# Kernel optimization log

Measured on AMD Instinct MI355X. Metric: run time of the kernel, lower is better.

The kernel has to match this reference:

```python
import jax, jax.numpy as jnp
import numpy as np

DIM = 1024
HEADS = 16
HEAD_DIM = DIM // HEADS
SCALE = HEAD_DIM ** -0.5
EPS_R = 1e-8
EPS_LN = 1e-5


def setup_inputs() -> dict:
    key = jax.random.key(0)
    ks = jax.random.split(key, 8)
    B, L = 4, 2048
    tokens = jax.random.normal(ks[0], (B, L, DIM), dtype=jnp.float32)
    R = jax.random.uniform(ks[1], (L, L), dtype=jnp.float32)
    s = DIM ** -0.5
    Wq = jax.random.normal(ks[2], (DIM, DIM), dtype=jnp.float32) * s
    Wk = jax.random.normal(ks[3], (DIM, DIM), dtype=jnp.float32) * s
    Wv = jax.random.normal(ks[4], (DIM, DIM), dtype=jnp.float32) * s
    Wp = jax.random.normal(ks[5], (DIM, DIM), dtype=jnp.float32) * s
    beta = jnp.ones((1,), dtype=jnp.float32)
    gamma = jnp.ones((DIM,), dtype=jnp.float32)
    bias = jnp.zeros((DIM,), dtype=jnp.float32)
    return {"tokens": tokens, "R": R, "Wq": Wq, "Wk": Wk, "Wv": Wv,
            "Wp": Wp, "beta": beta, "gamma": gamma, "bias": bias}


def reference(tokens, R, Wq, Wk, Wv, Wp, beta, gamma, bias):
    B, L, D = tokens.shape
    H, Dh = HEADS, HEAD_DIM
    residual = tokens
    # nn.Linear(bias=False): y = x @ W.T
    Q = (tokens @ Wq.T).reshape(B, L, H, Dh).transpose(0, 2, 1, 3)  # [B,H,L,Dh]
    K = (tokens @ Wk.T).reshape(B, L, H, Dh).transpose(0, 2, 1, 3)
    V = (tokens @ Wv.T).reshape(B, L, H, Dh).transpose(0, 2, 1, 3)
    attn = jnp.einsum('bhqd,bhkd->bhqk', Q, K) * SCALE
    log_R = jnp.log(jnp.maximum(R, EPS_R))  # [L,L]
    attn = attn + beta[0] * log_R[None, None, :, :]
    attn = jax.nn.softmax(attn, axis=-1)
    out = jnp.einsum('bhqk,bhkd->bhqd', attn, V)
    out = out.transpose(0, 2, 1, 3).reshape(B, L, D)
    out = out @ Wp.T
    x = out + residual
    mu = jnp.mean(x, axis=-1, keepdims=True)
    var = jnp.mean(jnp.square(x - mu), axis=-1, keepdims=True)
    return (x - mu) * jax.lax.rsqrt(var + EPS_LN) * gamma + bias
```

## Files before the change

kernel.cpp:

```cpp
#include <hip/hip_runtime.h>

#define DEV __device__ __forceinline__

typedef __attribute__((ext_vector_type(2))) float f32x2;
typedef __attribute__((ext_vector_type(4))) float f32x4;
typedef __attribute__((ext_vector_type(16))) float f32x16;
typedef __attribute__((ext_vector_type(8))) short bf8v;
typedef __attribute__((ext_vector_type(4))) unsigned short u16x4;
typedef __attribute__((ext_vector_type(8))) unsigned short u16x8;
typedef __attribute__((ext_vector_type(2))) unsigned int u32x2;
typedef __attribute__((ext_vector_type(4))) unsigned int u32x4;

static constexpr int LSEQ = 2048;
static constexpr int DIM  = 1024;
static constexpr int NH   = 16;
static constexpr int DH   = 64;
static constexpr int NB   = 4;
static constexpr int MROWS = NB * LSEQ;
static constexpr float QSCALE = 0.18033688011112042f;

DEV unsigned short f2bf(float x) {
  unsigned u = __float_as_uint(x);
  return (unsigned short)((u + 0x7fffu + ((u >> 16) & 1u)) >> 16);
}

DEV unsigned cvt_pk_bf16(float a, float b) {
  unsigned r;
  asm("v_cvt_pk_bf16_f32 %0, %1, %2" : "=v"(r) : "v"(a), "v"(b));
  return r;
}

DEV void pl32swap(unsigned& a, unsigned& b) {
  asm("v_permlane32_swap_b32 %0, %1" : "+v"(a), "+v"(b));
}

DEV float fexp2(float x) {
  float r;
  asm("v_exp_f32 %0, %1" : "=v"(r) : "v"(x));
  return r;
}

DEV void gload_lds16(const void* g, void* l) {
  __builtin_amdgcn_global_load_lds((const __attribute__((address_space(1))) void*)g,
                                   (__attribute__((address_space(3))) void*)l, 16, 0, 0);
}

__global__ __launch_bounds__(256) void k_cvt(const float* __restrict__ src,
                                             unsigned short* __restrict__ dst, int n) {
  int i = (blockIdx.x * 256 + threadIdx.x) * 8;
  if (i >= n) return;
  f32x4 a = *(const f32x4*)(src + i);
  f32x4 b = *(const f32x4*)(src + i + 4);
  u16x8 o;
  o[0] = f2bf(a[0]); o[1] = f2bf(a[1]); o[2] = f2bf(a[2]); o[3] = f2bf(a[3]);
  o[4] = f2bf(b[0]); o[5] = f2bf(b[1]); o[6] = f2bf(b[2]); o[7] = f2bf(b[3]);
  *(u16x8*)(dst + i) = o;
}

__global__ __launch_bounds__(256) void k_cvtw(const float* __restrict__ w0,
                                              const float* __restrict__ w1,
                                              const float* __restrict__ w2,
                                              const float* __restrict__ w3,
                                              unsigned short* __restrict__ dst) {
  int r = blockIdx.x >> 9;
  const float* src = (r == 0) ? w0 : (r == 1) ? w1 : (r == 2) ? w2 : w3;
  int i = ((blockIdx.x & 511) * 256 + threadIdx.x) * 8;
  f32x4 a = *(const f32x4*)(src + i);
  f32x4 b = *(const f32x4*)(src + i + 4);
  u16x8 o;
  o[0] = f2bf(a[0]); o[1] = f2bf(a[1]); o[2] = f2bf(a[2]); o[3] = f2bf(a[3]);
  o[4] = f2bf(b[0]); o[5] = f2bf(b[1]); o[6] = f2bf(b[2]); o[7] = f2bf(b[3]);
  *(u16x8*)(dst + (size_t)r * DIM * DIM + i) = o;
}

__global__ __launch_bounds__(256) void k_rbx(const float* __restrict__ R,
                                             const float* __restrict__ beta,
                                             u16x4* __restrict__ out) {
  __shared__ u16x4 lds2[2048];
  const int tid = threadIdx.x;
  const int q0 = blockIdx.x * 128;
  const int t  = blockIdx.y;
  const float b = beta[0];
  #pragma unroll
  for (int it = 0; it < 4; ++it) {
    int ql = it * 32 + (tid >> 3);
    int kl = (tid & 7) * 8;
    const float* src = R + (size_t)(q0 + ql) * 2048 + t * 64 + kl;
    f32x4 v0 = *(const f32x4*)src;
    f32x4 v1 = *(const f32x4*)(src + 4);
    u16x4 qa, qb;
    #pragma unroll
    for (int m = 0; m < 4; ++m) {
      qa[m] = f2bf(exp2f(b * log2f(fmaxf(v0[m], 1e-8f))));
      qb[m] = f2bf(exp2f(b * log2f(fmaxf(v1[m], 1e-8f))));
    }
    int s = kl >> 4, w = (kl >> 3) & 1;
    lds2[(((s * 2 + 0) * 128) + ql) * 2 + w] = qa;
    lds2[(((s * 2 + 1) * 128) + ql) * 2 + w] = qb;
  }
  __syncthreads();
  u16x8* O = (u16x8*)out;
  #pragma unroll
  for (int j = 0; j < 4; ++j) {
    int f = j * 256 + tid;
    int r = f >> 7, qrel = f & 127;
    O[(size_t)(t * 8 + r) * 2048 + q0 + qrel] = *(const u16x8*)&lds2[(r * 128 + qrel) * 2];
  }
}

DEV void gemm_core(const unsigned short* __restrict__ A, const unsigned short* __restrict__ Bm,
                   int m0, int n0, unsigned short* As, unsigned short* Bs, f32x4 (*acc)[4]) {
  const int tid = threadIdx.x;
  const int lane = tid & 63, wid = tid >> 6;
  const int g = lane >> 4, lq = lane & 15;
  const int wr = wid >> 1, wc = wid & 1;

  int aoff[2][4], boff[2][4];
  #pragma unroll
  for (int kk = 0; kk < 2; ++kk) {
    #pragma unroll
    for (int t = 0; t < 4; ++t) {
      aoff[kk][t] = (((wr * 64 + t * 16 + lq) * 128 + kk * 64 + g * 16) ^ ((lq & 7) << 4));
      boff[kk][t] = (((wc * 64 + t * 16 + lq) * 128 + kk * 64 + g * 16) ^ ((lq & 7) << 4));
    }
  }

  for (int kt = 0; kt < 16; ++kt) {
    #pragma unroll
    for (int i = 0; i < 4; ++i) {
      int chunk = i * 256 + tid;
      int row = chunk >> 3;
      int cc = (chunk & 7) ^ (row & 7);
      gload_lds16(A + (size_t)(m0 + row) * 1024 + kt * 64 + cc * 8, As + (i * 256 + wid * 64) * 8);
      gload_lds16(Bm + (size_t)(n0 + row) * 1024 + kt * 64 + cc * 8, Bs + (i * 256 + wid * 64) * 8);
    }
    __syncthreads();
    #pragma unroll
    for (int kk = 0; kk < 2; ++kk) {
      bf8v af[4], bfr[4];
      #pragma unroll
      for (int mi = 0; mi < 4; ++mi) af[mi] = *(const bf8v*)((const char*)As + aoff[kk][mi]);
      #pragma unroll
      for (int ni = 0; ni < 4; ++ni) bfr[ni] = *(const bf8v*)((const char*)Bs + boff[kk][ni]);
      #pragma unroll
      for (int mi = 0; mi < 4; ++mi)
        #pragma unroll
        for (int ni = 0; ni < 4; ++ni)
          acc[mi][ni] = __builtin_amdgcn_mfma_f32_16x16x32_bf16(af[mi], bfr[ni], acc[mi][ni], 0, 0, 0);
    }
    __syncthreads();
  }
}

__global__ __launch_bounds__(256) void k_gemm_qkv(
    const unsigned short* __restrict__ A, const unsigned short* __restrict__ W,
    unsigned short* __restrict__ Qb, unsigned short* __restrict__ Kb,
    unsigned short* __restrict__ Vt) {
  __shared__ unsigned short As[128 * 64];
  __shared__ unsigned short Bs[128 * 64];
  f32x4 acc[4][4];
  f32x4 z = {0.f, 0.f, 0.f, 0.f};
  #pragma unroll
  for (int mi = 0; mi < 4; ++mi)
    #pragma unroll
    for (int ni = 0; ni < 4; ++ni) acc[mi][ni] = z;

  const int m0 = blockIdx.x * 128, n0 = blockIdx.y * 128;
  gemm_core(A, W, m0, n0, As, Bs, acc);

  const int tid = threadIdx.x;
  const int lane = tid & 63, wid = tid >> 6;
  const int g = lane >> 4, lq = lane & 15;
  const int wr = wid >> 1, wc = wid & 1;
  const int region = n0 >> 10;
  const int nrel0 = n0 & 1023;

  if (region < 2) {
    unsigned short* dst = (region == 0) ? Qb : Kb;
    const float sc = (region == 0) ? QSCALE : 1.0f;
    #pragma unroll
    for (int mi = 0; mi < 4; ++mi)
      #pragma unroll
      for (int ni = 0; ni < 4; ++ni) {
        int m = m0 + wr * 64 + mi * 16 + g * 4;
        int n = nrel0 + wc * 64 + ni * 16 + lq;
        int b = m >> 11, l = m & 2047;
        int h = n >> 6, d = n & 63;
        int base = ((b * NH + h) * LSEQ + l) * DH + d;
        #pragma unroll
        for (int r = 0; r < 4; ++r)
          dst[base + r * DH] = f2bf(acc[mi][ni][r] * sc);
      }
  } else {
    #pragma unroll
    for (int mi = 0; mi < 4; ++mi)
      #pragma unroll
      for (int ni = 0; ni < 4; ++ni) {
        int m = m0 + wr * 64 + mi * 16 + g * 4;
        int n = nrel0 + wc * 64 + ni * 16 + lq;
        int b = m >> 11, l = m & 2047;
        int h = n >> 6, d = n & 63;
        u16x4 pk;
        #pragma unroll
        for (int r = 0; r < 4; ++r) pk[r] = f2bf(acc[mi][ni][r]);
        *(u16x4*)(Vt + (size_t)((b * NH + h) * DH + d) * LSEQ + l) = pk;
      }
  }
}

__global__ __launch_bounds__(256, 4) void k_attn(
    const unsigned short* __restrict__ Qb, const unsigned short* __restrict__ Kb,
    const unsigned short* __restrict__ Vt, const unsigned short* __restrict__ RbX,
    unsigned short* __restrict__ AO) {
  __shared__ unsigned short Ks[2][64 * 64];
  __shared__ unsigned short Vs[2][64 * 64];
  const int tid = threadIdx.x;
  const int lane = tid & 63, wid = tid >> 6;
  const int l32 = lane & 31, hi = lane >> 5;
  const int bh = blockIdx.y;
  const int q0 = blockIdx.x * 128;
  const int b = bh >> 4, h = bh & 15;
  const char* Kbh = (const char*)(Kb + (size_t)bh * LSEQ * DH);
  const char* Vbh = (const char*)(Vt + (size_t)bh * DH * LSEQ);
  const int qw = q0 + wid * 32;
  const int q = qw + l32;

  const unsigned short* Qbh = Qb + (size_t)bh * LSEQ * DH;
  bf8v qf[4];
  #pragma unroll
  for (int s = 0; s < 4; ++s)
    qf[s] = *(const bf8v*)(Qbh + (size_t)q * DH + s * 16 + hi * 8);

  f32x16 oacc[2];
  #pragma unroll
  for (int db = 0; db < 2; ++db)
    #pragma unroll
    for (int r = 0; r < 16; ++r) oacc[db][r] = 0.f;
  float mrun = -__builtin_inff();
  float lrun = 0.f;

  const unsigned rb_off = (unsigned)(hi * 2048 + q) * 16u;
  int koff, voff, ldso;
  {
    int row = tid >> 3;
    int cc = (tid & 7) ^ (row & 7);
    koff = row * (DH * 2) + cc * 16;
    voff = row * (LSEQ * 2) + cc * 16;
    ldso = (wid * 64) * 16;
  }

  gload_lds16(Kbh + koff, (char*)Ks[0] + ldso);
  gload_lds16(Kbh + koff + 4096, (char*)Ks[0] + ldso + 4096);
  gload_lds16(Vbh + voff, (char*)Vs[0] + ldso);
  gload_lds16(Vbh + voff + 131072, (char*)Vs[0] + ldso + 4096);
  __syncthreads();

  auto TILE = [&](int t, int buf, bool pref) {
    const char* rb_t = (const char*)RbX + (size_t)t * 262144;
    u32x4 rrA = *(const u32x4*)(rb_t + rb_off);
    u32x4 rrB = *(const u32x4*)(rb_t + 65536 + rb_off);

    if (pref) {
      const char* Kt = Kbh + (size_t)(t + 1) * (64 * DH * 2);
      const char* Vn = Vbh + (size_t)(t + 1) * (64 * 2);
      gload_lds16(Kt + koff, (char*)Ks[buf ^ 1] + ldso);
      gload_lds16(Kt + koff + 4096, (char*)Ks[buf ^ 1] + ldso + 4096);
      gload_lds16(Vn + voff, (char*)Vs[buf ^ 1] + ldso);
      gload_lds16(Vn + voff + 131072, (char*)Vs[buf ^ 1] + ldso + 4096);
    }

    f32x16 sac[2];
    #pragma unroll
    for (int r = 0; r < 16; ++r) { sac[0][r] = 0.f; sac[1][r] = 0.f; }
    __builtin_amdgcn_s_setprio(1);
    #pragma unroll
    for (int s = 0; s < 4; ++s) {
      #pragma unroll
      for (int kb2 = 0; kb2 < 2; ++kb2) {
        int row = kb2 * 32 + l32;
        bf8v kf = *(const bf8v*)((const char*)Ks[buf] +
                   ((row * 128 + s * 32 + hi * 16) ^ ((row & 7) << 4)));
        sac[kb2] = __builtin_amdgcn_mfma_f32_32x32x16_bf16(kf, qf[s], sac[kb2], 0, 0, 0);
      }
    }
    __builtin_amdgcn_s_setprio(0);

    float mx;
    {
      float m8[8];
      #pragma unroll
      for (int j = 0; j < 8; ++j)
        m8[j] = fmaxf(fmaxf(sac[0][2 * j], sac[0][2 * j + 1]),
                      fmaxf(sac[1][2 * j], sac[1][2 * j + 1]));
      float m4a = fmaxf(m8[0], m8[1]), m4b = fmaxf(m8[2], m8[3]);
      float m4c = fmaxf(m8[4], m8[5]), m4d = fmaxf(m8[6], m8[7]);
      mx = fmaxf(fmaxf(m4a, m4b), fmaxf(m4c, m4d));
      mx = fmaxf(mx, __shfl_xor(mx, 32));
    }

    if (__any(mx > mrun + 8.f)) {
      float mnew = fmaxf(mrun, mx);
      float corr = fexp2(mrun - mnew);
      mrun = mnew;
      lrun *= corr;
      #pragma unroll
      for (int db = 0; db < 2; ++db)
        #pragma unroll
        for (int r = 0; r < 16; ++r) oacc[db][r] *= corr;
    }

    f32x2 m2; m2[0] = mrun; m2[1] = mrun;
    f32x2 ls2; ls2[0] = 0.f; ls2[1] = 0.f;

    auto SLICE = [&](int s, const u32x4& rv) {
      const int blk = s >> 1, r0 = 8 * (s & 1);
      unsigned w[4];
      #pragma unroll
      for (int i = 0; i < 4; ++i) {
        f32x2 sv; sv[0] = sac[blk][r0 + 2 * i]; sv[1] = sac[blk][r0 + 2 * i + 1];
        sv = sv - m2;
        f32x2 pe; pe[0] = fexp2(sv[0]); pe[1] = fexp2(sv[1]);
        f32x2 rf;
        rf[0] = __uint_as_float(rv[i] << 16);
        rf[1] = __uint_as_float(rv[i] & 0xffff0000u);
        pe = pe * rf;
        ls2 = ls2 + pe;
        w[i] = cvt_pk_bf16(pe[0], pe[1]);
      }
      pl32swap(w[0], w[2]);
      pl32swap(w[1], w[3]);
      union { unsigned u[4]; bf8v v; } pf;
      pf.u[0] = w[0]; pf.u[1] = w[1]; pf.u[2] = w[2]; pf.u[3] = w[3];
      #pragma unroll
      for (int db = 0; db < 2; ++db) {
        int row = db * 32 + l32;
        bf8v vf = *(const bf8v*)((const char*)Vs[buf] +
                   ((row * 128 + s * 32 + hi * 16) ^ ((row & 7) << 4)));
        oacc[db] = __builtin_amdgcn_mfma_f32_32x32x16_bf16(vf, pf.v, oacc[db], 0, 0, 0);
      }
    };
    SLICE(0, rrA);
    rrA = *(const u32x4*)(rb_t + 131072 + rb_off);
    SLICE(1, rrB);
    rrB = *(const u32x4*)(rb_t + 196608 + rb_off);
    SLICE(2, rrA);
    SLICE(3, rrB);
    float ls = ls2[0] + ls2[1];
    ls += __shfl_xor(ls, 32);
    lrun += ls;
    __syncthreads();
  };

  for (int tp = 0; tp < 16; ++tp) {
    TILE(2 * tp,     0, true);
    TILE(2 * tp + 1, 1, tp != 15);
  }

  float inv = 1.f / lrun;
  #pragma unroll
  for (int db = 0; db < 2; ++db)
    #pragma unroll
    for (int u = 0; u < 4; ++u) {
      u32x2 w;
      w[0] = cvt_pk_bf16(oacc[db][4 * u + 0] * inv, oacc[db][4 * u + 1] * inv);
      w[1] = cvt_pk_bf16(oacc[db][4 * u + 2] * inv, oacc[db][4 * u + 3] * inv);
      int d = db * 32 + u * 8 + hi * 4;
      *(u32x2*)(AO + (size_t)(b * LSEQ + q) * DIM + h * DH + d) = w;
    }
}

__global__ __launch_bounds__(256) void k_gemm_proj(
    const unsigned short* __restrict__ A, const unsigned short* __restrict__ W,
    const float* __restrict__ res, float* __restrict__ out) {
  __shared__ unsigned short As[128 * 64];
  __shared__ unsigned short Bs[128 * 64];
  f32x4 acc[4][4];
  f32x4 z = {0.f, 0.f, 0.f, 0.f};
  #pragma unroll
  for (int mi = 0; mi < 4; ++mi)
    #pragma unroll
    for (int ni = 0; ni < 4; ++ni) acc[mi][ni] = z;

  const int m0 = blockIdx.x * 128, n0 = blockIdx.y * 128;
  gemm_core(A, W, m0, n0, As, Bs, acc);

  const int tid = threadIdx.x;
  const int lane = tid & 63, wid = tid >> 6;
  const int g = lane >> 4, lq = lane & 15;
  const int wr = wid >> 1, wc = wid & 1;
  #pragma unroll
  for (int mi = 0; mi < 4; ++mi)
    #pragma unroll
    for (int ni = 0; ni < 4; ++ni) {
      int m = m0 + wr * 64 + mi * 16 + g * 4;
      int n = n0 + wc * 64 + ni * 16 + lq;
      #pragma unroll
      for (int r = 0; r < 4; ++r) {
        int idx = (m + r) * 1024 + n;
        out[idx] = acc[mi][ni][r] + res[idx];
      }
    }
}

__global__ __launch_bounds__(256) void k_ln(float* __restrict__ x,
                                            const float* __restrict__ gamma,
                                            const float* __restrict__ bias) {
  const int row = blockIdx.x;
  const int tid = threadIdx.x;
  float* xr = x + (size_t)row * 1024;
  f32x4 v = *(f32x4*)(xr + tid * 4);
  float s = v[0] + v[1] + v[2] + v[3];
  float ss = v[0] * v[0] + v[1] * v[1] + v[2] * v[2] + v[3] * v[3];
  #pragma unroll
  for (int off = 1; off < 64; off <<= 1) {
    s += __shfl_xor(s, off);
    ss += __shfl_xor(ss, off);
  }
  __shared__ float red[8];
  const int lane = tid & 63, wid = tid >> 6;
  if (lane == 0) { red[wid] = s; red[wid + 4] = ss; }
  __syncthreads();
  s = red[0] + red[1] + red[2] + red[3];
  ss = red[4] + red[5] + red[6] + red[7];
  float mu = s * (1.f / 1024.f);
  float var = ss * (1.f / 1024.f) - mu * mu;
  float rs = rsqrtf(var + 1e-5f);
  f32x4 gm = *(const f32x4*)(gamma + tid * 4);
  f32x4 bi = *(const f32x4*)(bias + tid * 4);
  f32x4 o;
  #pragma unroll
  for (int j = 0; j < 4; ++j) o[j] = (v[j] - mu) * rs * gm[j] + bi[j];
  *(f32x4*)(xr + tid * 4) = o;
}

extern "C" void kernel_launch(void* const* d_in, const int* in_sizes, int n_in,
                              void* d_out, int out_size, void* d_ws, size_t ws_size,
                              hipStream_t stream) {
  const float* tokens = (const float*)d_in[0];
  const float* R      = (const float*)d_in[1];
  const float* Wq     = (const float*)d_in[2];
  const float* Wk     = (const float*)d_in[3];
  const float* Wv     = (const float*)d_in[4];
  const float* Wp     = (const float*)d_in[5];
  const float* beta   = (const float*)d_in[6];
  const float* gamma  = (const float*)d_in[7];
  const float* bias   = (const float*)d_in[8];
  float* out = (float*)d_out;
  char* ws = (char*)d_ws;

  unsigned short* tok_bf = (unsigned short*)(ws);
  unsigned short* wqkv   = (unsigned short*)(ws + 16777216);
  unsigned short* wp     = (unsigned short*)(ws + 23068672);
  u16x4*          rbx    = (u16x4*)(ws + 25165824);
  unsigned short* qb     = (unsigned short*)(ws + 41943040);
  unsigned short* kb     = (unsigned short*)(ws + 58720256);
  unsigned short* vt     = (unsigned short*)(ws + 75497472);
  unsigned short* ao     = tok_bf;

  k_cvt<<<4096, 256, 0, stream>>>(tokens, tok_bf, MROWS * DIM);
  k_cvtw<<<2048, 256, 0, stream>>>(Wq, Wk, Wv, Wp, wqkv);
  k_rbx<<<dim3(16, 32), 256, 0, stream>>>(R, beta, rbx);

  k_gemm_qkv<<<dim3(64, 24), 256, 0, stream>>>(tok_bf, wqkv, qb, kb, vt);
  k_attn<<<dim3(16, 64), 256, 0, stream>>>(qb, kb, vt, (const unsigned short*)rbx, ao);
  k_gemm_proj<<<dim3(64, 8), 256, 0, stream>>>(ao, wp, tokens, out);
  k_ln<<<8192, 256, 0, stream>>>(out, gamma, bias);
}
```

Baseline: 235.4 us.

## Read K and V fragments directly from global memory instead of LDS staging

The attention kernel no longer stages K and V tiles into double-buffered shared memory with async global-to-LDS loads and block barriers. Each wave now loads its MFMA operand fragments straight from global memory, relying on L1/L2 caching for reuse across the four waves in a block. This removes the LDS traffic and the per-tile __syncthreads, but each K/V element is fetched by every wave, there is no explicit prefetch, and the V loads are strided across rows of length LSEQ, so exposed memory latency may rise.

```diff
diff --git a/kernel.cpp b/kernel.cpp
--- a/kernel.cpp
+++ b/kernel.cpp
@@ -212,8 +212,6 @@
     const unsigned short* __restrict__ Qb, const unsigned short* __restrict__ Kb,
     const unsigned short* __restrict__ Vt, const unsigned short* __restrict__ RbX,
     unsigned short* __restrict__ AO) {
-  __shared__ unsigned short Ks[2][64 * 64];
-  __shared__ unsigned short Vs[2][64 * 64];
   const int tid = threadIdx.x;
   const int lane = tid & 63, wid = tid >> 6;
   const int l32 = lane & 31, hi = lane >> 5;
@@ -240,34 +238,16 @@
   float lrun = 0.f;
 
   const unsigned rb_off = (unsigned)(hi * 2048 + q) * 16u;
-  int koff, voff, ldso;
-  {
-    int row = tid >> 3;
-    int cc = (tid & 7) ^ (row & 7);
-    koff = row * (DH * 2) + cc * 16;
-    voff = row * (LSEQ * 2) + cc * 16;
-    ldso = (wid * 64) * 16;
-  }
-
-  gload_lds16(Kbh + koff, (char*)Ks[0] + ldso);
-  gload_lds16(Kbh + koff + 4096, (char*)Ks[0] + ldso + 4096);
-  gload_lds16(Vbh + voff, (char*)Vs[0] + ldso);
-  gload_lds16(Vbh + voff + 131072, (char*)Vs[0] + ldso + 4096);
-  __syncthreads();
-
-  auto TILE = [&](int t, int buf, bool pref) {
+  const int koffl = l32 * 128 + hi * 16;
+  const int voffl = l32 * 4096 + hi * 16;
+
+  for (int t = 0; t < 32; ++t) {
     const char* rb_t = (const char*)RbX + (size_t)t * 262144;
     u32x4 rrA = *(const u32x4*)(rb_t + rb_off);
     u32x4 rrB = *(const u32x4*)(rb_t + 65536 + rb_off);
 
-    if (pref) {
-      const char* Kt = Kbh + (size_t)(t + 1) * (64 * DH * 2);
-      const char* Vn = Vbh + (size_t)(t + 1) * (64 * 2);
-      gload_lds16(Kt + koff, (char*)Ks[buf ^ 1] + ldso);
-      gload_lds16(Kt + koff + 4096, (char*)Ks[buf ^ 1] + ldso + 4096);
-      gload_lds16(Vn + voff, (char*)Vs[buf ^ 1] + ldso);
-      gload_lds16(Vn + voff + 131072, (char*)Vs[buf ^ 1] + ldso + 4096);
-    }
+    const char* Kt = Kbh + (size_t)t * 8192;
+    const char* Vn = Vbh + (size_t)t * 128;
 
     f32x16 sac[2];
     #pragma unroll
@@ -277,9 +257,7 @@
     for (int s = 0; s < 4; ++s) {
       #pragma unroll
       for (int kb2 = 0; kb2 < 2; ++kb2) {
-        int row = kb2 * 32 + l32;
-        bf8v kf = *(const bf8v*)((const char*)Ks[buf] +
-                   ((row * 128 + s * 32 + hi * 16) ^ ((row & 7) << 4)));
+        bf8v kf = *(const bf8v*)(Kt + kb2 * 4096 + koffl + s * 32);
         sac[kb2] = __builtin_amdgcn_mfma_f32_32x32x16_bf16(kf, qf[s], sac[kb2], 0, 0, 0);
       }
     }
@@ -333,9 +311,7 @@
       pf.u[0] = w[0]; pf.u[1] = w[1]; pf.u[2] = w[2]; pf.u[3] = w[3];
       #pragma unroll
       for (int db = 0; db < 2; ++db) {
-        int row = db * 32 + l32;
-        bf8v vf = *(const bf8v*)((const char*)Vs[buf] +
-                   ((row * 128 + s * 32 + hi * 16) ^ ((row & 7) << 4)));
+        bf8v vf = *(const bf8v*)(Vn + db * 131072 + voffl + s * 32);
         oacc[db] = __builtin_amdgcn_mfma_f32_32x32x16_bf16(vf, pf.v, oacc[db], 0, 0, 0);
       }
     };
@@ -348,12 +324,6 @@
     float ls = ls2[0] + ls2[1];
     ls += __shfl_xor(ls, 32);
     lrun += ls;
-    __syncthreads();
-  };
-
-  for (int tp = 0; tp < 16; ++tp) {
-    TILE(2 * tp,     0, true);
-    TILE(2 * tp + 1, 1, tp != 15);
   }
 
   float inv = 1.f / lrun;
```

Result: slower. 376.9 us (+60.1%).

## Remap block IDs for XCD-aware L2 locality and trim attention softmax overhead

Applied to the files above, without the earlier changes.

Block indices in the QKV GEMM, attention and projection kernels are remapped so that consecutive blocks, which are dispatched round-robin across the eight XCDs, share the same tiles of A/W or the same K/V head on one XCD's L2. In the attention inner loop, the first MFMA takes a zero accumulator constant instead of explicitly zeroed registers, the row max uses a max3 reduction tree, and the cross-half shuffle for the softmax denominator moves out of the per-tile loop to a single shuffle at the end. The remapping assumes the grid shapes stay fixed (64x24, 16x64, 64x8) and the XCD dispatch is round-robin.

```diff
diff --git a/kernel.cpp b/kernel.cpp
--- a/kernel.cpp
+++ b/kernel.cpp
@@ -39,6 +39,8 @@
   asm("v_exp_f32 %0, %1" : "=v"(r) : "v"(x));
   return r;
 }
+
+DEV float max3(float a, float b, float c) { return fmaxf(fmaxf(a, b), c); }
 
 DEV void gload_lds16(const void* g, void* l) {
   __builtin_amdgcn_global_load_lds((const __attribute__((address_space(1))) void*)g,
@@ -165,7 +167,9 @@
     #pragma unroll
     for (int ni = 0; ni < 4; ++ni) acc[mi][ni] = z;
 
-  const int m0 = blockIdx.x * 128, n0 = blockIdx.y * 128;
+  int flat = blockIdx.y * 64 + blockIdx.x;
+  int nid = (flat & 7) * 192 + (flat >> 3);
+  const int m0 = (nid & 63) * 128, n0 = (nid >> 6) * 128;
   gemm_core(A, W, m0, n0, As, Bs, acc);
 
   const int tid = threadIdx.x;
@@ -217,8 +221,10 @@
   const int tid = threadIdx.x;
   const int lane = tid & 63, wid = tid >> 6;
   const int l32 = lane & 31, hi = lane >> 5;
-  const int bh = blockIdx.y;
-  const int q0 = blockIdx.x * 128;
+  int flat = blockIdx.y * 16 + blockIdx.x;
+  int nid = (flat & 7) * 128 + (flat >> 3);
+  const int bh = nid >> 4;
+  const int q0 = (nid & 15) * 128;
   const int b = bh >> 4, h = bh & 15;
   const char* Kbh = (const char*)(Kb + (size_t)bh * LSEQ * DH);
   const char* Vbh = (const char*)(Vt + (size_t)bh * DH * LSEQ);
@@ -238,6 +244,9 @@
     for (int r = 0; r < 16; ++r) oacc[db][r] = 0.f;
   float mrun = -__builtin_inff();
   float lrun = 0.f;
+
+  const f32x16 kz = {0.f, 0.f, 0.f, 0.f, 0.f, 0.f, 0.f, 0.f,
+                     0.f, 0.f, 0.f, 0.f, 0.f, 0.f, 0.f, 0.f};
 
   const unsigned rb_off = (unsigned)(hi * 2048 + q) * 16u;
   int koff, voff, ldso;
@@ -270,11 +279,16 @@
     }
 
     f32x16 sac[2];
-    #pragma unroll
-    for (int r = 0; r < 16; ++r) { sac[0][r] = 0.f; sac[1][r] = 0.f; }
     __builtin_amdgcn_s_setprio(1);
-    #pragma unroll
-    for (int s = 0; s < 4; ++s) {
+    {
+      int r0 = l32, r1 = 32 + l32;
+      bf8v kf0 = *(const bf8v*)((const char*)Ks[buf] + ((r0 * 128 + hi * 16) ^ ((r0 & 7) << 4)));
+      bf8v kf1 = *(const bf8v*)((const char*)Ks[buf] + ((r1 * 128 + hi * 16) ^ ((r1 & 7) << 4)));
+      sac[0] = __builtin_amdgcn_mfma_f32_32x32x16_bf16(kf0, qf[0], kz, 0, 0, 0);
+      sac[1] = __builtin_amdgcn_mfma_f32_32x32x16_bf16(kf1, qf[0], kz, 0, 0, 0);
+    }
+    #pragma unroll
+    for (int s = 1; s < 4; ++s) {
       #pragma unroll
       for (int kb2 = 0; kb2 < 2; ++kb2) {
         int row = kb2 * 32 + l32;
@@ -287,14 +301,21 @@
 
     float mx;
     {
-      float m8[8];
-      #pragma unroll
-      for (int j = 0; j < 8; ++j)
-        m8[j] = fmaxf(fmaxf(sac[0][2 * j], sac[0][2 * j + 1]),
-                      fmaxf(sac[1][2 * j], sac[1][2 * j + 1]));
-      float m4a = fmaxf(m8[0], m8[1]), m4b = fmaxf(m8[2], m8[3]);
-      float m4c = fmaxf(m8[4], m8[5]), m4d = fmaxf(m8[6], m8[7]);
-      mx = fmaxf(fmaxf(m4a, m4b), fmaxf(m4c, m4d));
+      float c0 = max3(sac[0][0], sac[0][1], sac[0][2]);
+      float c1 = max3(sac[0][4], sac[0][5], sac[0][6]);
+      float c2 = max3(sac[0][8], sac[0][9], sac[0][10]);
+      float c3 = max3(sac[0][12], sac[0][13], sac[0][14]);
+      c0 = max3(c0, sac[0][3], sac[1][0]);
+      c1 = max3(c1, sac[0][7], sac[1][4]);
+      c2 = max3(c2, sac[0][11], sac[1][8]);
+      c3 = max3(c3, sac[0][15], sac[1][12]);
+      c0 = max3(c0, sac[1][1], sac[1][2]);
+      c1 = max3(c1, sac[1][5], sac[1][6]);
+      c2 = max3(c2, sac[1][9], sac[1][10]);
+      c3 = max3(c3, sac[1][13], sac[1][14]);
+      c0 = max3(c0, sac[1][3], c1);
+      c2 = max3(c2, sac[1][7], c3);
+      mx = max3(c0, c2, fmaxf(sac[1][11], sac[1][15]));
       mx = fmaxf(mx, __shfl_xor(mx, 32));
     }
 
@@ -345,9 +366,7 @@
     rrB = *(const u32x4*)(rb_t + 196608 + rb_off);
     SLICE(2, rrA);
     SLICE(3, rrB);
-    float ls = ls2[0] + ls2[1];
-    ls += __shfl_xor(ls, 32);
-    lrun += ls;
+    lrun += ls2[0] + ls2[1];
     __syncthreads();
   };
 
@@ -356,6 +375,7 @@
     TILE(2 * tp + 1, 1, tp != 15);
   }
 
+  lrun += __shfl_xor(lrun, 32);
   float inv = 1.f / lrun;
   #pragma unroll
   for (int db = 0; db < 2; ++db)
@@ -381,7 +401,9 @@
     #pragma unroll
     for (int ni = 0; ni < 4; ++ni) acc[mi][ni] = z;
 
-  const int m0 = blockIdx.x * 128, n0 = blockIdx.y * 128;
+  int flat = blockIdx.y * 64 + blockIdx.x;
+  int nid = (flat & 7) * 64 + (flat >> 3);
+  const int m0 = (nid & 63) * 128, n0 = (nid >> 6) * 128;
   gemm_core(A, W, m0, n0, As, Bs, acc);
 
   const int tid = threadIdx.x;
```

Result: slower. 243.2 us (+3.3%).
